# Kernel tuning notes

Measured on AMD Instinct MI355X. Metric: run time of the kernel, lower is better.

## Reference

```python
import jax, jax.numpy as jnp
import numpy as np

IN_CH = 384
HEAD_DIM = 32
MAX_SEQ = 64          # P, tokens per window
N_HEADS = IN_CH // HEAD_DIM
PART = int(np.sqrt(MAX_SEQ))  # 8, window side
SCALE = HEAD_DIM ** -0.5


def _relative_position_index():
    # Swin relative position index, [P*P] int
    h = np.arange(PART)
    coords = np.stack(np.meshgrid(h, h, indexing='ij')).reshape(2, -1)  # [2, P]
    rel = coords[:, :, None] - coords[:, None, :]                        # [2, P, P]
    rel = rel.transpose(1, 2, 0).astype(np.int64)
    rel[:, :, 0] += PART - 1
    rel[:, :, 1] += PART - 1
    rel[:, :, 0] *= 2 * PART - 1
    return rel.sum(-1).reshape(-1)  # [P*P]

REL_IDX = jnp.asarray(_relative_position_index())


def setup_inputs() -> dict:
    key = jax.random.key(0)
    ks = jax.random.split(key, 6)
    B, G, P, D = 32, 64, MAX_SEQ, IN_CH
    x = jax.random.normal(ks[0], (B, G, P, D), dtype=jnp.float32)
    Wqkv = jax.random.normal(ks[1], (D, 3 * D), dtype=jnp.float32) * (D ** -0.5)
    bqkv = jnp.zeros((3 * D,), dtype=jnp.float32)
    Wm = jax.random.normal(ks[2], (D, D), dtype=jnp.float32) * (D ** -0.5)
    bm = jnp.zeros((D,), dtype=jnp.float32)
    # torch init is zeros; use small normal so bias actually affects the output
    rel_table = jax.random.normal(ks[3], ((2 * PART - 1) ** 2, N_HEADS), dtype=jnp.float32) * 0.02
    return {"x": x, "Wqkv": Wqkv, "bqkv": bqkv, "Wm": Wm, "bm": bm, "rel_table": rel_table}


def reference(x, Wqkv, bqkv, Wm, bm, rel_table):
    B, G, P, D = x.shape
    H, DH = N_HEADS, HEAD_DIM
    qkv = x @ Wqkv + bqkv                                   # [B,G,P,3D]
    q, k, v = jnp.split(qkv, 3, axis=-1)
    q = q.reshape(B, G, P, H, DH) * SCALE
    k = k.reshape(B, G, P, H, DH)
    v = v.reshape(B, G, P, H, DH)
    attn = jnp.einsum('bgihd,bgjhd->bghij', q, k)           # [B,G,H,P,P]
    bias = rel_table[REL_IDX].reshape(P, P, H).transpose(2, 0, 1)  # [H,P,P]
    attn = jax.nn.softmax(attn + bias[None, None], axis=-1)
    out = jnp.einsum('bghij,bgjhd->bgihd', attn, v)         # [B,G,P,H,DH]
    out = out.reshape(B, G, P, D)
    return out @ Wm + bm
```

## Files before the change

### kernel.cpp

```cpp
#include <hip/hip_runtime.h>
#include <stdint.h>


typedef __attribute__((ext_vector_type(4))) float f32x4;
typedef __attribute__((ext_vector_type(4))) short s16x4;
typedef __attribute__((ext_vector_type(8))) short s16x8;

#define DEVI static __device__ __forceinline__

DEVI unsigned short f2bf(float f) {
  union { float f; uint32_t u; } v; v.f = f;
  return (unsigned short)((v.u + 0x7FFFu + ((v.u >> 16) & 1u)) >> 16);
}

DEVI uint32_t pk2(float lo, float hi) {
  return (uint32_t)f2bf(lo) | ((uint32_t)f2bf(hi) << 16);
}

DEVI f32x4 zero4() { f32x4 z; z[0] = 0.f; z[1] = 0.f; z[2] = 0.f; z[3] = 0.f; return z; }

#if defined(__has_builtin)
#if __has_builtin(__builtin_amdgcn_mfma_f32_16x16x16bf16_1k)
#define MFMA16_BUILTIN 1
#endif
#if __has_builtin(__builtin_amdgcn_global_load_lds)
#define HAS_GLLDS 1
#endif
#endif

DEVI f32x4 mfma16(s16x4 a, s16x4 b, f32x4 c) {
#ifdef MFMA16_BUILTIN
  return __builtin_amdgcn_mfma_f32_16x16x16bf16_1k(a, b, c, 0, 0, 0);
#else
  asm volatile("v_mfma_f32_16x16x16_bf16 %0, %1, %2, %0" : "+v"(c) : "v"(a), "v"(b));
  return c;
#endif
}

DEVI f32x4 mfma32(s16x8 a, s16x8 b, f32x4 c) {
  return __builtin_amdgcn_mfma_f32_16x16x32_bf16(a, b, c, 0, 0, 0);
}

DEVI void stage1k(const unsigned short* g_lane, unsigned short* lds_base) {
#ifdef HAS_GLLDS
  __builtin_amdgcn_global_load_lds(
      (const __attribute__((address_space(1))) unsigned int*)g_lane,
      (__attribute__((address_space(3))) unsigned int*)lds_base, 16, 0, 0);
#else
  *(s16x8*)(lds_base + (threadIdx.x & 63) * 8) = *(const s16x8*)g_lane;
#endif
}

__global__ void fill_val(float* o, int n, float v) {
  int t = blockIdx.x * 256 + threadIdx.x;
  if (t < n) o[t] = v;
}

__global__ __launch_bounds__(256) void prep_all(
    const float* __restrict__ x, unsigned short* __restrict__ xb,
    const float* __restrict__ Wqkv, unsigned short* __restrict__ WqkvT,
    const float* __restrict__ Wm, unsigned short* __restrict__ WmT,
    const float* __restrict__ bqkv, float* __restrict__ bqkvs,
    const float* __restrict__ rel, float* __restrict__ biasF) {
  const int b = blockIdx.x;
  if (b < 2048) {
    const size_t nchunk = 131072UL * 384 / 8;
    for (size_t i = (size_t)b * 256 + threadIdx.x; i < nchunk; i += 2048UL * 256) {
      f32x4 a = *(const f32x4*)(x + i * 8);
      f32x4 c = *(const f32x4*)(x + i * 8 + 4);
      s16x8 p;
      p[0] = (short)f2bf(a[0]); p[1] = (short)f2bf(a[1]);
      p[2] = (short)f2bf(a[2]); p[3] = (short)f2bf(a[3]);
      p[4] = (short)f2bf(c[0]); p[5] = (short)f2bf(c[1]);
      p[6] = (short)f2bf(c[2]); p[7] = (short)f2bf(c[3]);
      *(s16x8*)(xb + i * 8) = p;
    }
  } else if (b == 2048) {
    for (int t = threadIdx.x; t < 1152; t += 256)
      bqkvs[t] = bqkv[t] * ((t < 384) ? 0.17677669529663687f : 1.0f);
  } else if (b < 2097) {
    int t = (b - 2049) * 256 + threadIdx.x;
    if (t < 12288) {
      int h = t >> 10;
      int r = (t >> 6) & 15;
      int lane = t & 63;
      int jt = r >> 2, it = r & 3;
      int lg = lane >> 4, lr = lane & 15;
      int i = it * 16 + lr;
#pragma unroll
      for (int e = 0; e < 4; ++e) {
        int j = jt * 16 + lg * 4 + e;
        int idx = ((i >> 3) - (j >> 3) + 7) * 15 + ((i & 7) - (j & 7) + 7);
        biasF[t * 4 + e] = rel[idx * 12 + h];
      }
    }
  } else if (b < 2673) {
    int t = (b - 2097) * 256 + threadIdx.x;
    int n = t / 384, k = t - n * 384;
    WmT[t] = f2bf(Wm[(size_t)k * 384 + n]);
  } else {
    int t = (b - 2673) * 256 + threadIdx.x;
    int n = t / 384, k = t - n * 384;
    float s = (n < 384) ? 0.17677669529663687f : 1.0f;
    WqkvT[t] = f2bf(Wqkv[(size_t)k * 1152 + n] * s);
  }
}

template <bool QKV_EPI>
__global__ __launch_bounds__(512, 4) void gemm_k(const unsigned short* __restrict__ A,
                                                 const unsigned short* __restrict__ BT,
                                                 const float* __restrict__ bias,
                                                 void* __restrict__ Cv) {
  constexpr int K = 384;
  constexpr int NT = QKV_EPI ? 9 : 3;
  constexpr int N = NT * 128;
  __shared__ unsigned short sm[2][16384];
  const int bid = blockIdx.x;
  const int swz = (bid & 7) * (NT * 128) + (bid >> 3);
  const int n0 = (swz % NT) * 128;
  const int m0 = (swz / NT) * 128;
  const int tid = threadIdx.x;
  const int lane = tid & 63, wv = tid >> 6;
  const int wr = wv >> 2, wc = wv & 3;
  const int lg = lane >> 4, lr = lane & 15;

  const int scol = ((lane & 7) ^ (lane >> 3)) * 8;
  const unsigned short* Ag = A + (size_t)(m0 + wv * 16 + (lane >> 3)) * K + scol;
  const unsigned short* Bg = BT + (size_t)(n0 + wv * 16 + (lane >> 3)) * K + scol;

  f32x4 acc[4][2];
#pragma unroll
  for (int i = 0; i < 4; ++i)
#pragma unroll
    for (int j = 0; j < 2; ++j) acc[i][j] = zero4();

  auto STAGE = [&](int buf, int k0) {
#pragma unroll
    for (int c2 = 0; c2 < 2; ++c2)
      stage1k(Ag + (size_t)(c2 * 8) * K + k0, &sm[buf][(wv * 16 + c2 * 8) * 64]);
#pragma unroll
    for (int c2 = 0; c2 < 2; ++c2)
      stage1k(Bg + (size_t)(c2 * 8) * K + k0, &sm[buf][8192 + (wv * 16 + c2 * 8) * 64]);
  };
  const int sa = (lr & 7) << 3;
  auto COMPUTE = [&](int buf) {
#pragma unroll
    for (int kk = 0; kk < 64; kk += 32) {
      s16x8 af[4], bf[2];
#pragma unroll
      for (int mt = 0; mt < 4; ++mt)
        af[mt] = *(const s16x8*)&sm[buf][(wr * 64 + 16 * mt + lr) * 64 + ((kk + 8 * lg) ^ sa)];
#pragma unroll
      for (int nt = 0; nt < 2; ++nt)
        bf[nt] = *(const s16x8*)&sm[buf][8192 + (wc * 32 + 16 * nt + lr) * 64 + ((kk + 8 * lg) ^ sa)];
#pragma unroll
      for (int mt = 0; mt < 4; ++mt)
#pragma unroll
        for (int nt = 0; nt < 2; ++nt)
          acc[mt][nt] = mfma32(af[mt], bf[nt], acc[mt][nt]);
    }
  };

  STAGE(0, 0);
  int cur = 0;
#pragma unroll 1
  for (int t = 0; t < 5; ++t) {
    STAGE(cur ^ 1, (t + 1) * 64);
    asm volatile("s_waitcnt vmcnt(4)" ::: "memory");
    __builtin_amdgcn_sched_barrier(0);
    __builtin_amdgcn_s_barrier();
    __builtin_amdgcn_sched_barrier(0);
    COMPUTE(cur);
    __builtin_amdgcn_sched_barrier(0);
    __builtin_amdgcn_s_barrier();
    cur ^= 1;
  }
  asm volatile("s_waitcnt vmcnt(0)" ::: "memory");
  __builtin_amdgcn_sched_barrier(0);
  __builtin_amdgcn_s_barrier();
  __builtin_amdgcn_sched_barrier(0);
  COMPUTE(cur);

  const int crow = m0 + wr * 64 + 4 * lg;
  const int ccol = n0 + wc * 32 + lr;
  if constexpr (QKV_EPI) {
    const int sel = n0 / 384;
    unsigned short* qkv = (unsigned short*)Cv;
    if (sel < 2) {
      unsigned short* tile = &sm[0][0];
#pragma unroll
      for (int nt = 0; nt < 2; ++nt) {
        const int cc = wc * 32 + 16 * nt + lr;
        const float bv = bias[n0 + cc];
#pragma unroll
        for (int mt = 0; mt < 4; ++mt) {
#pragma unroll
          for (int e = 0; e < 4; ++e) {
            const int r = wr * 64 + 16 * mt + 4 * lg + e;
            tile[r * 128 + (cc ^ ((r & 7) << 3))] = f2bf(acc[mt][nt][e] + bv);
          }
        }
      }
      __syncthreads();
      const int hbase = (n0 - sel * 384) >> 5;
      const int tr = wv * 16 + (lane >> 2);
      const int gtok = m0 + tr;
      const int w2 = gtok >> 6, t0r = gtok & 63;
#pragma unroll
      for (int hh = 0; hh < 4; ++hh) {
        const int chunk = hh * 4 + (lane & 3);
        s16x8 v = *(const s16x8*)&tile[tr * 128 + ((chunk * 8) ^ ((tr & 7) << 3))];
        unsigned short* dst = qkv + (((size_t)w2 * 12 + hbase + hh) * 3 + sel) * 2048 +
                              t0r * 32 + (lane & 3) * 8;
        *(s16x8*)dst = v;
      }
    } else {
      const int window = crow >> 6;
      const int t0 = crow & 63;
#pragma unroll
      for (int nt = 0; nt < 2; ++nt) {
        const int col = ccol + 16 * nt;
        const int hcol = col - 768;
        const int h = hcol >> 5, d = hcol & 31;
        const float bv = bias[col];
        unsigned short* base = qkv + (((size_t)window * 12 + h) * 3 + 2) * 2048;
#pragma unroll
        for (int mt = 0; mt < 4; ++mt) {
          s16x4 pk;
#pragma unroll
          for (int e = 0; e < 4; ++e) pk[e] = (short)f2bf(acc[mt][nt][e] + bv);
          *(s16x4*)&base[d * 64 + t0 + 16 * mt] = pk;
        }
      }
    }
  } else {
    float* C = (float*)Cv;
#pragma unroll
    for (int mt = 0; mt < 4; ++mt)
#pragma unroll
      for (int nt = 0; nt < 2; ++nt) {
        const int col = ccol + 16 * nt;
        const float bv = bias[col];
#pragma unroll
        for (int e = 0; e < 4; ++e)
          C[(size_t)(crow + 16 * mt + e) * N + col] = acc[mt][nt][e] + bv;
      }
  }
}

__global__ __launch_bounds__(768) void attn_gemm2_k(const unsigned short* __restrict__ qkv,
                                                    const float* __restrict__ biasF,
                                                    const unsigned short* __restrict__ WmT,
                                                    const float* __restrict__ bm,
                                                    float* __restrict__ out) {
  __shared__ unsigned short att_s[64 * 392];
  const int lane = threadIdx.x & 63;
  const int wv = threadIdx.x >> 6;
  const int window = blockIdx.x;
  const int h = wv;
  const int lg = lane >> 4, lr = lane & 15;

  const unsigned short* hb = qkv + ((size_t)window * 12 + h) * 6144;
  const unsigned short* Qh = hb;
  const unsigned short* Kh = hb + 2048;
  const unsigned short* Vth = hb + 4096;

  s16x8 ka[4], qb[4];
#pragma unroll
  for (int jt = 0; jt < 4; ++jt)
    ka[jt] = *(const s16x8*)&Kh[(jt * 16 + lr) * 32 + 8 * lg];
#pragma unroll
  for (int it = 0; it < 4; ++it)
    qb[it] = *(const s16x8*)&Qh[(it * 16 + lr) * 32 + 8 * lg];

  f32x4 c[4][4];
#pragma unroll
  for (int a = 0; a < 4; ++a)
#pragma unroll
    for (int b2 = 0; b2 < 4; ++b2) c[a][b2] = zero4();

#pragma unroll
  for (int jt = 0; jt < 4; ++jt)
#pragma unroll
    for (int it = 0; it < 4; ++it)
      c[jt][it] = mfma32(ka[jt], qb[it], c[jt][it]);

  const f32x4* bF = (const f32x4*)biasF + ((size_t)h * 16) * 64 + lane;
#pragma unroll
  for (int jt = 0; jt < 4; ++jt)
#pragma unroll
    for (int it = 0; it < 4; ++it)
      c[jt][it] += bF[(jt * 4 + it) * 64];

  s16x4 pb[4][4];
#pragma unroll
  for (int it = 0; it < 4; ++it) {
    float m = -3.0e38f;
#pragma unroll
    for (int jt = 0; jt < 4; ++jt)
#pragma unroll
      for (int e = 0; e < 4; ++e) m = fmaxf(m, c[jt][it][e]);
    m = fmaxf(m, __shfl_xor(m, 16));
    m = fmaxf(m, __shfl_xor(m, 32));
    float s = 0.f;
#pragma unroll
    for (int jt = 0; jt < 4; ++jt)
#pragma unroll
      for (int e = 0; e < 4; ++e) {
        float p = __expf(c[jt][it][e] - m);
        c[jt][it][e] = p;
        s += p;
      }
    s += __shfl_xor(s, 16);
    s += __shfl_xor(s, 32);
    const float inv = 1.f / s;
#pragma unroll
    for (int jt = 0; jt < 4; ++jt) {
      s16x4 pk;
#pragma unroll
      for (int e = 0; e < 4; ++e) pk[e] = (short)f2bf(c[jt][it][e] * inv);
      pb[jt][it] = pk;
    }
  }

  f32x4 o[2][4];
#pragma unroll
  for (int a = 0; a < 2; ++a)
#pragma unroll
    for (int b2 = 0; b2 < 4; ++b2) o[a][b2] = zero4();

#pragma unroll
  for (int jt = 0; jt < 4; ++jt) {
    s16x4 va[2];
#pragma unroll
    for (int dt = 0; dt < 2; ++dt)
      va[dt] = *(const s16x4*)&Vth[(dt * 16 + lr) * 64 + jt * 16 + 4 * lg];
#pragma unroll
    for (int dt = 0; dt < 2; ++dt)
#pragma unroll
      for (int it = 0; it < 4; ++it)
        o[dt][it] = mfma16(va[dt], pb[jt][it], o[dt][it]);
  }

#pragma unroll
  for (int it = 0; it < 4; ++it) {
    const uint32_t p0 = pk2(o[0][it][0], o[0][it][1]);
    const uint32_t p1 = pk2(o[0][it][2], o[0][it][3]);
    const uint32_t q0 = pk2(o[1][it][0], o[1][it][1]);
    const uint32_t q1 = pk2(o[1][it][2], o[1][it][3]);

    const uint32_t x16_0 = __shfl_xor((int)(lg == 2 ? q0 : p0), 16);
    const uint32_t x16_1 = __shfl_xor((int)(lg == 2 ? q1 : p1), 16);
    const uint32_t x32_0 = __shfl_xor((int)(lg == 0 ? q0 : p0), 32);
    const uint32_t x32_1 = __shfl_xor((int)(lg == 0 ? q1 : p1), 32);
    const uint32_t x48_0 = __shfl_xor((int)(lg == 1 ? q0 : p0), 48);
    const uint32_t x48_1 = __shfl_xor((int)(lg == 1 ? q1 : p1), 48);

    uint32_t w[4];
    w[0] = lg == 0 ? p0 : lg == 1 ? x48_0 : lg == 2 ? x32_0 : x16_0;
    w[1] = lg == 0 ? p1 : lg == 1 ? x48_1 : lg == 2 ? x32_1 : x16_1;
    w[2] = lg == 0 ? x16_0 : lg == 1 ? x32_0 : lg == 2 ? x48_0 : q0;
    w[3] = lg == 0 ? x16_1 : lg == 1 ? x32_1 : lg == 2 ? x48_1 : q1;

    *(uint4*)&att_s[(size_t)(it * 16 + lr) * 392 + h * 32 + 8 * lg] =
        make_uint4(w[0], w[1], w[2], w[3]);
  }

  __syncthreads();

  f32x4 acc[4][2];
#pragma unroll
  for (int mt = 0; mt < 4; ++mt)
#pragma unroll
    for (int nt = 0; nt < 2; ++nt) acc[mt][nt] = zero4();

  const int n0w = wv * 32;
#pragma unroll 2
  for (int ks = 0; ks < 12; ++ks) {
    s16x8 af[4], bf[2];
#pragma unroll
    for (int mt = 0; mt < 4; ++mt)
      af[mt] = *(const s16x8*)&att_s[(16 * mt + lr) * 392 + ks * 32 + 8 * lg];
#pragma unroll
    for (int nt = 0; nt < 2; ++nt)
      bf[nt] = *(const s16x8*)&WmT[(size_t)(n0w + 16 * nt + lr) * 384 + ks * 32 + 8 * lg];
#pragma unroll
    for (int mt = 0; mt < 4; ++mt)
#pragma unroll
      for (int nt = 0; nt < 2; ++nt)
        acc[mt][nt] = mfma32(af[mt], bf[nt], acc[mt][nt]);
  }

  float* ob = out + (size_t)window * 64 * 384;
#pragma unroll
  for (int mt = 0; mt < 4; ++mt)
#pragma unroll
    for (int nt = 0; nt < 2; ++nt) {
      const int col = n0w + 16 * nt + lr;
      const float bv = bm[col];
#pragma unroll
      for (int e = 0; e < 4; ++e)
        ob[(size_t)(16 * mt + 4 * lg + e) * 384 + col] = acc[mt][nt][e] + bv;
    }
}

extern "C" void kernel_launch(void* const* d_in, const int* in_sizes, int n_in,
                              void* d_out, int out_size, void* d_ws, size_t ws_size,
                              hipStream_t stream) {
  const float* x = (const float*)d_in[0];
  const float* Wqkv = (const float*)d_in[1];
  const float* bqkv = (const float*)d_in[2];
  const float* Wm = (const float*)d_in[3];
  const float* bm = (const float*)d_in[4];
  const float* rel = (const float*)d_in[5];

  const size_t M = 131072;
  char* ws = (char*)d_ws;
  size_t off = 0;
  unsigned short* qkv = (unsigned short*)(ws + off);   off += M * 1152 * 2;
  unsigned short* xb = (unsigned short*)(ws + off);    off += M * 384 * 2;
  unsigned short* WqkvT = (unsigned short*)(ws + off); off += 1152 * 384 * 2;
  unsigned short* WmT = (unsigned short*)(ws + off);   off += 384 * 384 * 2;
  float* biasF = (float*)(ws + off);                   off += 12 * 16 * 64 * 4 * 4;
  float* bqkvs = (float*)(ws + off);                   off += 1152 * 4;

  if (ws_size < off) {
    fill_val<<<(out_size + 255) / 256, 256, 0, stream>>>((float*)d_out, out_size, 12345.0f);
    return;
  }

  prep_all<<<4401, 256, 0, stream>>>(x, xb, Wqkv, WqkvT, Wm, WmT, bqkv, bqkvs, rel, biasF);
  gemm_k<true><<<9216, 512, 0, stream>>>(xb, WqkvT, bqkvs, qkv);
  attn_gemm2_k<<<2048, 768, 0, stream>>>(qkv, biasF, WmT, bm, (float*)d_out);
}
```

Measured before the change: 424.8 us.

## Fuse QKV projection into per-window attention kernel, drop qkv intermediate

```diff
diff --git a/kernel.cpp b/kernel.cpp
--- a/kernel.cpp
+++ b/kernel.cpp
@@ -106,172 +106,109 @@
   }
 }
 
-template <bool QKV_EPI>
-__global__ __launch_bounds__(512, 4) void gemm_k(const unsigned short* __restrict__ A,
-                                                 const unsigned short* __restrict__ BT,
-                                                 const float* __restrict__ bias,
-                                                 void* __restrict__ Cv) {
-  constexpr int K = 384;
-  constexpr int NT = QKV_EPI ? 9 : 3;
-  constexpr int N = NT * 128;
-  __shared__ unsigned short sm[2][16384];
-  const int bid = blockIdx.x;
-  const int swz = (bid & 7) * (NT * 128) + (bid >> 3);
-  const int n0 = (swz % NT) * 128;
-  const int m0 = (swz / NT) * 128;
-  const int tid = threadIdx.x;
-  const int lane = tid & 63, wv = tid >> 6;
-  const int wr = wv >> 2, wc = wv & 3;
-  const int lg = lane >> 4, lr = lane & 15;
-
-  const int scol = ((lane & 7) ^ (lane >> 3)) * 8;
-  const unsigned short* Ag = A + (size_t)(m0 + wv * 16 + (lane >> 3)) * K + scol;
-  const unsigned short* Bg = BT + (size_t)(n0 + wv * 16 + (lane >> 3)) * K + scol;
-
-  f32x4 acc[4][2];
-#pragma unroll
-  for (int i = 0; i < 4; ++i)
-#pragma unroll
-    for (int j = 0; j < 2; ++j) acc[i][j] = zero4();
-
-  auto STAGE = [&](int buf, int k0) {
-#pragma unroll
-    for (int c2 = 0; c2 < 2; ++c2)
-      stage1k(Ag + (size_t)(c2 * 8) * K + k0, &sm[buf][(wv * 16 + c2 * 8) * 64]);
-#pragma unroll
-    for (int c2 = 0; c2 < 2; ++c2)
-      stage1k(Bg + (size_t)(c2 * 8) * K + k0, &sm[buf][8192 + (wv * 16 + c2 * 8) * 64]);
-  };
-  const int sa = (lr & 7) << 3;
-  auto COMPUTE = [&](int buf) {
-#pragma unroll
-    for (int kk = 0; kk < 64; kk += 32) {
-      s16x8 af[4], bf[2];
-#pragma unroll
-      for (int mt = 0; mt < 4; ++mt)
-        af[mt] = *(const s16x8*)&sm[buf][(wr * 64 + 16 * mt + lr) * 64 + ((kk + 8 * lg) ^ sa)];
-#pragma unroll
-      for (int nt = 0; nt < 2; ++nt)
-        bf[nt] = *(const s16x8*)&sm[buf][8192 + (wc * 32 + 16 * nt + lr) * 64 + ((kk + 8 * lg) ^ sa)];
-#pragma unroll
-      for (int mt = 0; mt < 4; ++mt)
-#pragma unroll
-        for (int nt = 0; nt < 2; ++nt)
-          acc[mt][nt] = mfma32(af[mt], bf[nt], acc[mt][nt]);
-    }
-  };
-
-  STAGE(0, 0);
-  int cur = 0;
-#pragma unroll 1
-  for (int t = 0; t < 5; ++t) {
-    STAGE(cur ^ 1, (t + 1) * 64);
-    asm volatile("s_waitcnt vmcnt(4)" ::: "memory");
-    __builtin_amdgcn_sched_barrier(0);
-    __builtin_amdgcn_s_barrier();
-    __builtin_amdgcn_sched_barrier(0);
-    COMPUTE(cur);
-    __builtin_amdgcn_sched_barrier(0);
-    __builtin_amdgcn_s_barrier();
-    cur ^= 1;
-  }
-  asm volatile("s_waitcnt vmcnt(0)" ::: "memory");
-  __builtin_amdgcn_sched_barrier(0);
-  __builtin_amdgcn_s_barrier();
-  __builtin_amdgcn_sched_barrier(0);
-  COMPUTE(cur);
-
-  const int crow = m0 + wr * 64 + 4 * lg;
-  const int ccol = n0 + wc * 32 + lr;
-  if constexpr (QKV_EPI) {
-    const int sel = n0 / 384;
-    unsigned short* qkv = (unsigned short*)Cv;
-    if (sel < 2) {
-      unsigned short* tile = &sm[0][0];
-#pragma unroll
-      for (int nt = 0; nt < 2; ++nt) {
-        const int cc = wc * 32 + 16 * nt + lr;
-        const float bv = bias[n0 + cc];
-#pragma unroll
-        for (int mt = 0; mt < 4; ++mt) {
-#pragma unroll
-          for (int e = 0; e < 4; ++e) {
-            const int r = wr * 64 + 16 * mt + 4 * lg + e;
-            tile[r * 128 + (cc ^ ((r & 7) << 3))] = f2bf(acc[mt][nt][e] + bv);
-          }
-        }
-      }
-      __syncthreads();
-      const int hbase = (n0 - sel * 384) >> 5;
-      const int tr = wv * 16 + (lane >> 2);
-      const int gtok = m0 + tr;
-      const int w2 = gtok >> 6, t0r = gtok & 63;
-#pragma unroll
-      for (int hh = 0; hh < 4; ++hh) {
-        const int chunk = hh * 4 + (lane & 3);
-        s16x8 v = *(const s16x8*)&tile[tr * 128 + ((chunk * 8) ^ ((tr & 7) << 3))];
-        unsigned short* dst = qkv + (((size_t)w2 * 12 + hbase + hh) * 3 + sel) * 2048 +
-                              t0r * 32 + (lane & 3) * 8;
-        *(s16x8*)dst = v;
-      }
-    } else {
-      const int window = crow >> 6;
-      const int t0 = crow & 63;
-#pragma unroll
-      for (int nt = 0; nt < 2; ++nt) {
-        const int col = ccol + 16 * nt;
-        const int hcol = col - 768;
-        const int h = hcol >> 5, d = hcol & 31;
-        const float bv = bias[col];
-        unsigned short* base = qkv + (((size_t)window * 12 + h) * 3 + 2) * 2048;
-#pragma unroll
-        for (int mt = 0; mt < 4; ++mt) {
-          s16x4 pk;
-#pragma unroll
-          for (int e = 0; e < 4; ++e) pk[e] = (short)f2bf(acc[mt][nt][e] + bv);
-          *(s16x4*)&base[d * 64 + t0 + 16 * mt] = pk;
-        }
-      }
-    }
-  } else {
-    float* C = (float*)Cv;
-#pragma unroll
-    for (int mt = 0; mt < 4; ++mt)
-#pragma unroll
-      for (int nt = 0; nt < 2; ++nt) {
-        const int col = ccol + 16 * nt;
-        const float bv = bias[col];
-#pragma unroll
-        for (int e = 0; e < 4; ++e)
-          C[(size_t)(crow + 16 * mt + e) * N + col] = acc[mt][nt][e] + bv;
-      }
-  }
-}
-
-__global__ __launch_bounds__(768) void attn_gemm2_k(const unsigned short* __restrict__ qkv,
-                                                    const float* __restrict__ biasF,
-                                                    const unsigned short* __restrict__ WmT,
-                                                    const float* __restrict__ bm,
-                                                    float* __restrict__ out) {
-  __shared__ unsigned short att_s[64 * 392];
+__global__ __launch_bounds__(768) void fused_k(const unsigned short* __restrict__ xb,
+                                               const unsigned short* __restrict__ WqkvT,
+                                               const float* __restrict__ bqkvs,
+                                               const float* __restrict__ biasF,
+                                               const unsigned short* __restrict__ WmT,
+                                               const float* __restrict__ bm,
+                                               float* __restrict__ out) {
+  __shared__ __attribute__((aligned(16))) unsigned short smem[49664];
+  unsigned short* x_s = smem;
+  unsigned short* qks = smem;
+  unsigned short* att_s = smem;
+
   const int lane = threadIdx.x & 63;
   const int wv = threadIdx.x >> 6;
   const int window = blockIdx.x;
-  const int h = wv;
   const int lg = lane >> 4, lr = lane & 15;
 
-  const unsigned short* hb = qkv + ((size_t)window * 12 + h) * 6144;
-  const unsigned short* Qh = hb;
-  const unsigned short* Kh = hb + 2048;
-  const unsigned short* Vth = hb + 4096;
+  for (int r = wv; r < 64; r += 12) {
+    const unsigned short* src =
+        xb + (size_t)(window * 64 + r) * 384 + (size_t)((lane ^ (r & 7)) * 8);
+    stage1k(src, &x_s[r * 512]);
+  }
+  __syncthreads();
+
+#define AF(mt, ks) \
+  (*(const s16x8*)&x_s[(16 * (mt) + lr) * 512 + (((ks) * 4 + lg) ^ (lr & 7)) * 8])
+
+  f32x4 accv[4][2];
+#pragma unroll
+  for (int mt = 0; mt < 4; ++mt)
+#pragma unroll
+    for (int nt = 0; nt < 2; ++nt) accv[mt][nt] = zero4();
+  {
+    const unsigned short* W0 = WqkvT + (size_t)(768 + wv * 32 + lr) * 384 + 8 * lg;
+    const unsigned short* W1 = W0 + (size_t)16 * 384;
+#pragma unroll
+    for (int ks = 0; ks < 12; ++ks) {
+      s16x8 bf0 = *(const s16x8*)(W0 + ks * 32);
+      s16x8 bf1 = *(const s16x8*)(W1 + ks * 32);
+#pragma unroll
+      for (int mt = 0; mt < 4; ++mt) {
+        s16x8 a = AF(mt, ks);
+        accv[mt][0] = mfma32(a, bf0, accv[mt][0]);
+        accv[mt][1] = mfma32(a, bf1, accv[mt][1]);
+      }
+    }
+  }
+  s16x4 va[4][2];
+#pragma unroll
+  for (int dt = 0; dt < 2; ++dt) {
+    const float bv = bqkvs[768 + wv * 32 + dt * 16 + lr];
+#pragma unroll
+    for (int jt = 0; jt < 4; ++jt) {
+      s16x4 pk;
+#pragma unroll
+      for (int e = 0; e < 4; ++e) pk[e] = (short)f2bf(accv[jt][dt][e] + bv);
+      va[jt][dt] = pk;
+    }
+  }
+
+  f32x4 acck[4][4];
+#pragma unroll
+  for (int mt = 0; mt < 4; ++mt)
+#pragma unroll
+    for (int nt = 0; nt < 4; ++nt) acck[mt][nt] = zero4();
+  {
+    const unsigned short* Wq = WqkvT + (size_t)(wv * 64 + lr) * 384 + 8 * lg;
+#pragma unroll
+    for (int ks = 0; ks < 12; ++ks) {
+      s16x8 bf[4];
+#pragma unroll
+      for (int nt = 0; nt < 4; ++nt)
+        bf[nt] = *(const s16x8*)(Wq + (size_t)(16 * nt) * 384 + ks * 32);
+#pragma unroll
+      for (int mt = 0; mt < 4; ++mt) {
+        s16x8 a = AF(mt, ks);
+#pragma unroll
+        for (int nt = 0; nt < 4; ++nt) acck[mt][nt] = mfma32(a, bf[nt], acck[mt][nt]);
+      }
+    }
+  }
+  __syncthreads();
+
+#pragma unroll
+  for (int nt = 0; nt < 4; ++nt) {
+    const int qkcol = wv * 64 + 16 * nt + lr;
+    const float bv = bqkvs[qkcol];
+#pragma unroll
+    for (int mt = 0; mt < 4; ++mt)
+#pragma unroll
+      for (int e = 0; e < 4; ++e)
+        qks[(16 * mt + 4 * lg + e) * 776 + qkcol] = f2bf(acck[mt][nt][e] + bv);
+  }
+  __syncthreads();
 
   s16x8 ka[4], qb[4];
 #pragma unroll
   for (int jt = 0; jt < 4; ++jt)
-    ka[jt] = *(const s16x8*)&Kh[(jt * 16 + lr) * 32 + 8 * lg];
+    ka[jt] = *(const s16x8*)&qks[(16 * jt + lr) * 776 + 384 + wv * 32 + 8 * lg];
 #pragma unroll
   for (int it = 0; it < 4; ++it)
-    qb[it] = *(const s16x8*)&Qh[(it * 16 + lr) * 32 + 8 * lg];
+    qb[it] = *(const s16x8*)&qks[(16 * it + lr) * 776 + wv * 32 + 8 * lg];
+  __syncthreads();
 
   f32x4 c[4][4];
 #pragma unroll
@@ -285,7 +222,7 @@
     for (int it = 0; it < 4; ++it)
       c[jt][it] = mfma32(ka[jt], qb[it], c[jt][it]);
 
-  const f32x4* bF = (const f32x4*)biasF + ((size_t)h * 16) * 64 + lane;
+  const f32x4* bF = (const f32x4*)biasF + ((size_t)wv * 16) * 64 + lane;
 #pragma unroll
   for (int jt = 0; jt < 4; ++jt)
 #pragma unroll
@@ -330,17 +267,12 @@
     for (int b2 = 0; b2 < 4; ++b2) o[a][b2] = zero4();
 
 #pragma unroll
-  for (int jt = 0; jt < 4; ++jt) {
-    s16x4 va[2];
+  for (int jt = 0; jt < 4; ++jt)
 #pragma unroll
     for (int dt = 0; dt < 2; ++dt)
-      va[dt] = *(const s16x4*)&Vth[(dt * 16 + lr) * 64 + jt * 16 + 4 * lg];
-#pragma unroll
-    for (int dt = 0; dt < 2; ++dt)
 #pragma unroll
       for (int it = 0; it < 4; ++it)
-        o[dt][it] = mfma16(va[dt], pb[jt][it], o[dt][it]);
-  }
+        o[dt][it] = mfma16(va[jt][dt], pb[jt][it], o[dt][it]);
 
 #pragma unroll
   for (int it = 0; it < 4; ++it) {
@@ -362,7 +294,7 @@
     w[2] = lg == 0 ? x16_0 : lg == 1 ? x32_0 : lg == 2 ? x48_0 : q0;
     w[3] = lg == 0 ? x16_1 : lg == 1 ? x32_1 : lg == 2 ? x48_1 : q1;
 
-    *(uint4*)&att_s[(size_t)(it * 16 + lr) * 392 + h * 32 + 8 * lg] =
+    *(uint4*)&att_s[(size_t)(it * 16 + lr) * 392 + wv * 32 + 8 * lg] =
         make_uint4(w[0], w[1], w[2], w[3]);
   }
 
@@ -402,6 +334,7 @@
       for (int e = 0; e < 4; ++e)
         ob[(size_t)(16 * mt + 4 * lg + e) * 384 + col] = acc[mt][nt][e] + bv;
     }
+#undef AF
 }
 
 extern "C" void kernel_launch(void* const* d_in, const int* in_sizes, int n_in,
@@ -417,12 +350,12 @@
   const size_t M = 131072;
   char* ws = (char*)d_ws;
   size_t off = 0;
-  unsigned short* qkv = (unsigned short*)(ws + off);   off += M * 1152 * 2;
   unsigned short* xb = (unsigned short*)(ws + off);    off += M * 384 * 2;
   unsigned short* WqkvT = (unsigned short*)(ws + off); off += 1152 * 384 * 2;
   unsigned short* WmT = (unsigned short*)(ws + off);   off += 384 * 384 * 2;
   float* biasF = (float*)(ws + off);                   off += 12 * 16 * 64 * 4 * 4;
   float* bqkvs = (float*)(ws + off);                   off += 1152 * 4;
+  off += 1024;
 
   if (ws_size < off) {
     fill_val<<<(out_size + 255) / 256, 256, 0, stream>>>((float*)d_out, out_size, 12345.0f);
@@ -430,6 +363,5 @@
   }
 
   prep_all<<<4401, 256, 0, stream>>>(x, xb, Wqkv, WqkvT, Wm, WmT, bqkv, bqkvs, rel, biasF);
-  gemm_k<true><<<9216, 512, 0, stream>>>(xb, WqkvT, bqkvs, qkv);
-  attn_gemm2_k<<<2048, 768, 0, stream>>>(qkv, biasF, WmT, bm, (float*)d_out);
-}
+  fused_k<<<2048, 768, 0, stream>>>(xb, WqkvT, bqkvs, biasF, WmT, bm, (float*)d_out);
+}
```

Measured after the change: 693.0 us. +63.1%, slower.

## Halve attention block to 6 waves, each wave handling two heads

Applied to the files above, without the earlier changes.

```diff
diff --git a/kernel.cpp b/kernel.cpp
--- a/kernel.cpp
+++ b/kernel.cpp
@@ -248,160 +248,172 @@
   }
 }
 
-__global__ __launch_bounds__(768) void attn_gemm2_k(const unsigned short* __restrict__ qkv,
-                                                    const float* __restrict__ biasF,
-                                                    const unsigned short* __restrict__ WmT,
-                                                    const float* __restrict__ bm,
-                                                    float* __restrict__ out) {
+__global__ __launch_bounds__(384, 5) void attn_gemm2_k(const unsigned short* __restrict__ qkv,
+                                                       const float* __restrict__ biasF,
+                                                       const unsigned short* __restrict__ WmT,
+                                                       const float* __restrict__ bm,
+                                                       float* __restrict__ out) {
   __shared__ unsigned short att_s[64 * 392];
   const int lane = threadIdx.x & 63;
   const int wv = threadIdx.x >> 6;
   const int window = blockIdx.x;
-  const int h = wv;
   const int lg = lane >> 4, lr = lane & 15;
 
-  const unsigned short* hb = qkv + ((size_t)window * 12 + h) * 6144;
-  const unsigned short* Qh = hb;
-  const unsigned short* Kh = hb + 2048;
-  const unsigned short* Vth = hb + 4096;
-
-  s16x8 ka[4], qb[4];
-#pragma unroll
-  for (int jt = 0; jt < 4; ++jt)
-    ka[jt] = *(const s16x8*)&Kh[(jt * 16 + lr) * 32 + 8 * lg];
-#pragma unroll
-  for (int it = 0; it < 4; ++it)
-    qb[it] = *(const s16x8*)&Qh[(it * 16 + lr) * 32 + 8 * lg];
-
-  f32x4 c[4][4];
-#pragma unroll
-  for (int a = 0; a < 4; ++a)
-#pragma unroll
-    for (int b2 = 0; b2 < 4; ++b2) c[a][b2] = zero4();
-
-#pragma unroll
-  for (int jt = 0; jt < 4; ++jt)
-#pragma unroll
-    for (int it = 0; it < 4; ++it)
-      c[jt][it] = mfma32(ka[jt], qb[it], c[jt][it]);
-
-  const f32x4* bF = (const f32x4*)biasF + ((size_t)h * 16) * 64 + lane;
-#pragma unroll
-  for (int jt = 0; jt < 4; ++jt)
-#pragma unroll
-    for (int it = 0; it < 4; ++it)
-      c[jt][it] += bF[(jt * 4 + it) * 64];
-
-  s16x4 pb[4][4];
-#pragma unroll
-  for (int it = 0; it < 4; ++it) {
-    float m = -3.0e38f;
+#pragma unroll 1
+  for (int hp = 0; hp < 2; ++hp) {
+    const int h = wv * 2 + hp;
+    const unsigned short* hb = qkv + ((size_t)window * 12 + h) * 6144;
+    const unsigned short* Qh = hb;
+    const unsigned short* Kh = hb + 2048;
+    const unsigned short* Vth = hb + 4096;
+
+    s16x8 ka[4];
 #pragma unroll
     for (int jt = 0; jt < 4; ++jt)
-#pragma unroll
-      for (int e = 0; e < 4; ++e) m = fmaxf(m, c[jt][it][e]);
-    m = fmaxf(m, __shfl_xor(m, 16));
-    m = fmaxf(m, __shfl_xor(m, 32));
-    float s = 0.f;
-#pragma unroll
-    for (int jt = 0; jt < 4; ++jt)
-#pragma unroll
-      for (int e = 0; e < 4; ++e) {
-        float p = __expf(c[jt][it][e] - m);
-        c[jt][it][e] = p;
-        s += p;
-      }
-    s += __shfl_xor(s, 16);
-    s += __shfl_xor(s, 32);
-    const float inv = 1.f / s;
-#pragma unroll
-    for (int jt = 0; jt < 4; ++jt) {
-      s16x4 pk;
-#pragma unroll
-      for (int e = 0; e < 4; ++e) pk[e] = (short)f2bf(c[jt][it][e] * inv);
-      pb[jt][it] = pk;
-    }
-  }
-
-  f32x4 o[2][4];
-#pragma unroll
-  for (int a = 0; a < 2; ++a)
-#pragma unroll
-    for (int b2 = 0; b2 < 4; ++b2) o[a][b2] = zero4();
-
-#pragma unroll
-  for (int jt = 0; jt < 4; ++jt) {
-    s16x4 va[2];
-#pragma unroll
-    for (int dt = 0; dt < 2; ++dt)
-      va[dt] = *(const s16x4*)&Vth[(dt * 16 + lr) * 64 + jt * 16 + 4 * lg];
-#pragma unroll
-    for (int dt = 0; dt < 2; ++dt)
-#pragma unroll
-      for (int it = 0; it < 4; ++it)
-        o[dt][it] = mfma16(va[dt], pb[jt][it], o[dt][it]);
-  }
-
-#pragma unroll
-  for (int it = 0; it < 4; ++it) {
-    const uint32_t p0 = pk2(o[0][it][0], o[0][it][1]);
-    const uint32_t p1 = pk2(o[0][it][2], o[0][it][3]);
-    const uint32_t q0 = pk2(o[1][it][0], o[1][it][1]);
-    const uint32_t q1 = pk2(o[1][it][2], o[1][it][3]);
-
-    const uint32_t x16_0 = __shfl_xor((int)(lg == 2 ? q0 : p0), 16);
-    const uint32_t x16_1 = __shfl_xor((int)(lg == 2 ? q1 : p1), 16);
-    const uint32_t x32_0 = __shfl_xor((int)(lg == 0 ? q0 : p0), 32);
-    const uint32_t x32_1 = __shfl_xor((int)(lg == 0 ? q1 : p1), 32);
-    const uint32_t x48_0 = __shfl_xor((int)(lg == 1 ? q0 : p0), 48);
-    const uint32_t x48_1 = __shfl_xor((int)(lg == 1 ? q1 : p1), 48);
-
-    uint32_t w[4];
-    w[0] = lg == 0 ? p0 : lg == 1 ? x48_0 : lg == 2 ? x32_0 : x16_0;
-    w[1] = lg == 0 ? p1 : lg == 1 ? x48_1 : lg == 2 ? x32_1 : x16_1;
-    w[2] = lg == 0 ? x16_0 : lg == 1 ? x32_0 : lg == 2 ? x48_0 : q0;
-    w[3] = lg == 0 ? x16_1 : lg == 1 ? x32_1 : lg == 2 ? x48_1 : q1;
-
-    *(uint4*)&att_s[(size_t)(it * 16 + lr) * 392 + h * 32 + 8 * lg] =
-        make_uint4(w[0], w[1], w[2], w[3]);
+      ka[jt] = *(const s16x8*)&Kh[(jt * 16 + lr) * 32 + 8 * lg];
+
+#pragma unroll 1
+    for (int itp = 0; itp < 2; ++itp) {
+      s16x8 qb[2];
+#pragma unroll
+      for (int i2 = 0; i2 < 2; ++i2)
+        qb[i2] = *(const s16x8*)&Qh[((itp * 2 + i2) * 16 + lr) * 32 + 8 * lg];
+
+      f32x4 c[4][2];
+#pragma unroll
+      for (int a = 0; a < 4; ++a)
+#pragma unroll
+        for (int b2 = 0; b2 < 2; ++b2) c[a][b2] = zero4();
+
+#pragma unroll
+      for (int jt = 0; jt < 4; ++jt)
+#pragma unroll
+        for (int i2 = 0; i2 < 2; ++i2)
+          c[jt][i2] = mfma32(ka[jt], qb[i2], c[jt][i2]);
+
+      const f32x4* bF = (const f32x4*)biasF + ((size_t)h * 16) * 64 + lane;
+#pragma unroll
+      for (int jt = 0; jt < 4; ++jt)
+#pragma unroll
+        for (int i2 = 0; i2 < 2; ++i2)
+          c[jt][i2] += bF[(jt * 4 + itp * 2 + i2) * 64];
+
+      s16x4 pb[4][2];
+#pragma unroll
+      for (int i2 = 0; i2 < 2; ++i2) {
+        float m = -3.0e38f;
+#pragma unroll
+        for (int jt = 0; jt < 4; ++jt)
+#pragma unroll
+          for (int e = 0; e < 4; ++e) m = fmaxf(m, c[jt][i2][e]);
+        m = fmaxf(m, __shfl_xor(m, 16));
+        m = fmaxf(m, __shfl_xor(m, 32));
+        float s = 0.f;
+#pragma unroll
+        for (int jt = 0; jt < 4; ++jt)
+#pragma unroll
+          for (int e = 0; e < 4; ++e) {
+            float p = __expf(c[jt][i2][e] - m);
+            c[jt][i2][e] = p;
+            s += p;
+          }
+        s += __shfl_xor(s, 16);
+        s += __shfl_xor(s, 32);
+        const float inv = 1.f / s;
+#pragma unroll
+        for (int jt = 0; jt < 4; ++jt) {
+          s16x4 pk;
+#pragma unroll
+          for (int e = 0; e < 4; ++e) pk[e] = (short)f2bf(c[jt][i2][e] * inv);
+          pb[jt][i2] = pk;
+        }
+      }
+
+      f32x4 o[2][2];
+#pragma unroll
+      for (int a = 0; a < 2; ++a)
+#pragma unroll
+        for (int b2 = 0; b2 < 2; ++b2) o[a][b2] = zero4();
+
+#pragma unroll
+      for (int jt = 0; jt < 4; ++jt) {
+        s16x4 va[2];
+#pragma unroll
+        for (int dt = 0; dt < 2; ++dt)
+          va[dt] = *(const s16x4*)&Vth[(dt * 16 + lr) * 64 + jt * 16 + 4 * lg];
+#pragma unroll
+        for (int dt = 0; dt < 2; ++dt)
+#pragma unroll
+          for (int i2 = 0; i2 < 2; ++i2)
+            o[dt][i2] = mfma16(va[dt], pb[jt][i2], o[dt][i2]);
+      }
+
+#pragma unroll
+      for (int i2 = 0; i2 < 2; ++i2) {
+        const int it = itp * 2 + i2;
+        const uint32_t p0 = pk2(o[0][i2][0], o[0][i2][1]);
+        const uint32_t p1 = pk2(o[0][i2][2], o[0][i2][3]);
+        const uint32_t q0 = pk2(o[1][i2][0], o[1][i2][1]);
+        const uint32_t q1 = pk2(o[1][i2][2], o[1][i2][3]);
+
+        const uint32_t x16_0 = __shfl_xor((int)(lg == 2 ? q0 : p0), 16);
+        const uint32_t x16_1 = __shfl_xor((int)(lg == 2 ? q1 : p1), 16);
+        const uint32_t x32_0 = __shfl_xor((int)(lg == 0 ? q0 : p0), 32);
+        const uint32_t x32_1 = __shfl_xor((int)(lg == 0 ? q1 : p1), 32);
+        const uint32_t x48_0 = __shfl_xor((int)(lg == 1 ? q0 : p0), 48);
+        const uint32_t x48_1 = __shfl_xor((int)(lg == 1 ? q1 : p1), 48);
+
+        uint32_t w[4];
+        w[0] = lg == 0 ? p0 : lg == 1 ? x48_0 : lg == 2 ? x32_0 : x16_0;
+        w[1] = lg == 0 ? p1 : lg == 1 ? x48_1 : lg == 2 ? x32_1 : x16_1;
+        w[2] = lg == 0 ? x16_0 : lg == 1 ? x32_0 : lg == 2 ? x48_0 : q0;
+        w[3] = lg == 0 ? x16_1 : lg == 1 ? x32_1 : lg == 2 ? x48_1 : q1;
+
+        *(uint4*)&att_s[(size_t)(it * 16 + lr) * 392 + h * 32 + 8 * lg] =
+            make_uint4(w[0], w[1], w[2], w[3]);
+      }
+    }
   }
 
   __syncthreads();
 
-  f32x4 acc[4][2];
-#pragma unroll
-  for (int mt = 0; mt < 4; ++mt)
-#pragma unroll
-    for (int nt = 0; nt < 2; ++nt) acc[mt][nt] = zero4();
-
-  const int n0w = wv * 32;
+  float* ob = out + (size_t)window * 64 * 384;
+#pragma unroll 1
+  for (int np = 0; np < 2; ++np) {
+    const int n0w = wv * 64 + np * 32;
+    f32x4 acc[4][2];
+#pragma unroll
+    for (int mt = 0; mt < 4; ++mt)
+#pragma unroll
+      for (int nt = 0; nt < 2; ++nt) acc[mt][nt] = zero4();
+
 #pragma unroll 2
-  for (int ks = 0; ks < 12; ++ks) {
-    s16x8 af[4], bf[2];
+    for (int ks = 0; ks < 12; ++ks) {
+      s16x8 af[4], bf[2];
+#pragma unroll
+      for (int mt = 0; mt < 4; ++mt)
+        af[mt] = *(const s16x8*)&att_s[(16 * mt + lr) * 392 + ks * 32 + 8 * lg];
+#pragma unroll
+      for (int nt = 0; nt < 2; ++nt)
+        bf[nt] = *(const s16x8*)&WmT[(size_t)(n0w + 16 * nt + lr) * 384 + ks * 32 + 8 * lg];
+#pragma unroll
+      for (int mt = 0; mt < 4; ++mt)
+#pragma unroll
+        for (int nt = 0; nt < 2; ++nt)
+          acc[mt][nt] = mfma32(af[mt], bf[nt], acc[mt][nt]);
+    }
+
 #pragma unroll
     for (int mt = 0; mt < 4; ++mt)
-      af[mt] = *(const s16x8*)&att_s[(16 * mt + lr) * 392 + ks * 32 + 8 * lg];
-#pragma unroll
-    for (int nt = 0; nt < 2; ++nt)
-      bf[nt] = *(const s16x8*)&WmT[(size_t)(n0w + 16 * nt + lr) * 384 + ks * 32 + 8 * lg];
-#pragma unroll
-    for (int mt = 0; mt < 4; ++mt)
-#pragma unroll
-      for (int nt = 0; nt < 2; ++nt)
-        acc[mt][nt] = mfma32(af[mt], bf[nt], acc[mt][nt]);
-  }
-
-  float* ob = out + (size_t)window * 64 * 384;
-#pragma unroll
-  for (int mt = 0; mt < 4; ++mt)
-#pragma unroll
-    for (int nt = 0; nt < 2; ++nt) {
-      const int col = n0w + 16 * nt + lr;
-      const float bv = bm[col];
-#pragma unroll
-      for (int e = 0; e < 4; ++e)
-        ob[(size_t)(16 * mt + 4 * lg + e) * 384 + col] = acc[mt][nt][e] + bv;
-    }
+#pragma unroll
+      for (int nt = 0; nt < 2; ++nt) {
+        const int col = n0w + 16 * nt + lr;
+        const float bv = bm[col];
+#pragma unroll
+        for (int e = 0; e < 4; ++e)
+          ob[(size_t)(16 * mt + 4 * lg + e) * 384 + col] = acc[mt][nt][e] + bv;
+      }
+  }
 }
 
 extern "C" void kernel_launch(void* const* d_in, const int* in_sizes, int n_in,
@@ -431,5 +443,5 @@
 
   prep_all<<<4401, 256, 0, stream>>>(x, xb, Wqkv, WqkvT, Wm, WmT, bqkv, bqkvs, rel, biasF);
   gemm_k<true><<<9216, 512, 0, stream>>>(xb, WqkvT, bqkvs, qkv);
-  attn_gemm2_k<<<2048, 768, 0, stream>>>(qkv, biasF, WmT, bm, (float*)d_out);
-}
+  attn_gemm2_k<<<2048, 384, 0, stream>>>(qkv, biasF, WmT, bm, (float*)d_out);
+}
```

Result: slower. 450.0 us (+5.9%).
